# Optimization experiments

Hardware: AMD Instinct MI355X
Metric: run time of the kernel (lower is better)

## Reference

```python
import jax, jax.numpy as jnp
import numpy as np

HRNN = 2e-11  # seconds per step; t grid is in nanoseconds (x1e9), step = 0.02
W0, W1 = -20.0, 10.0          # fixed oscillator coupling weights
X0 = (0.4736, 0.8745, 1.8497)  # fixed initial state


def setup_inputs() -> dict:
    key = jax.random.key(0)
    ks = jax.random.split(key, 9)
    B, T, NIN, NHI, NHO, NOUT = 1024, 2048, 8, 64, 64, 1
    g = lambda k, shape, s: jax.random.normal(k, shape, jnp.float32) * s
    return {
        "inputdata": jax.random.normal(ks[0], (B, T, NIN), jnp.float32),
        "Wni": g(ks[1], (NHI, NIN), 1.0 / np.sqrt(NIN)),   # nonlinearinput
        "bni": g(ks[2], (NHI,), 0.1),
        "Wli": g(ks[3], (1, NHI), 1.0 / np.sqrt(NHI)),     # linearinput
        "bli": g(ks[4], (1,), 0.1),
        "tau": jnp.zeros((1,), jnp.float32),                # nn.Parameter(Tensor(1))
        "Wn": g(ks[5], (NHO, 3), 1.0 / np.sqrt(3.0)),      # nonlinear readout
        "bn": g(ks[6], (NHO,), 0.1),
        "Wl": g(ks[7], (NOUT, NHO), 1.0 / np.sqrt(NHO)),   # linear readout
        "bl": g(ks[8], (NOUT,), 0.1),
    }


def reference(inputdata, Wni, bni, Wli, bli, tau, Wn, bn, Wl, bl):
    B, T, NIN = inputdata.shape
    tg = jnp.linspace(0.0, HRNN * (T - 1) * 1e9, T).astype(jnp.float32)
    u = inputdata  # [B, T, NIN]
    x0 = jnp.broadcast_to(jnp.array(X0, jnp.float32)[None, :], (B, 3))

    def lin_interp(t):
        # clamp-to-edge linear interpolation of u along the time grid
        ind = jnp.clip(jnp.searchsorted(tg, t), 1, T - 1)
        t_lo, t_hi = tg[ind - 1], tg[ind]
        frac = jnp.clip((t - t_lo) / (t_hi - t_lo), 0.0, 1.0)
        u_lo = u[:, ind - 1, :]
        return u_lo + (u[:, ind, :] - u_lo) * frac  # [B, NIN]

    def f(t, x):
        ut = lin_interp(t)
        dparam = jax.nn.sigmoid(ut @ Wni.T + bni) @ Wli.T + bli  # [B, 1]
        tx = jnp.tanh(x)
        dx = jnp.stack(
            (-x[:, 0] + tx[:, 1],
             -x[:, 1] + tx[:, 2],
             -x[:, 2] + W0 * tx[:, 0] + W1 * tx[:, 1]),
            axis=1,
        )
        return dx / jnp.exp(tau + dparam)  # [B, 3]

    def step(x, ts):
        # torchdiffeq 'rk4' = fourth-order 3/8 rule between grid points
        t0, t1 = ts
        h = t1 - t0
        k1 = f(t0, x)
        k2 = f(t0 + h / 3, x + h * k1 / 3)
        k3 = f(t0 + 2 * h / 3, x + h * (k2 - k1 / 3))
        k4 = f(t1, x + h * (k1 - k2 + k3))
        xn = x + h * (k1 + 3 * k2 + 3 * k3 + k4) / 8
        return xn, xn

    _, xs = jax.lax.scan(step, x0, (tg[:-1], tg[1:]))  # [T-1, B, 3]
    outrnn = jnp.concatenate([x0[None], xs], axis=0).transpose(1, 0, 2)  # [B, T, 3]
    hid = jax.nn.sigmoid(outrnn @ Wn.T + bn)  # [B, T, NHO]
    return hid @ Wl.T + bl  # [B, T, NOUT]
```

## Files before the change

### kernel.cpp

```cpp
#include <hip/hip_runtime.h>

#define BB 1024
#define TT 2048
#define NIN 8
#define NHI 64

#define CS 2.8853900817779268f
#define NL2E 1.4426950408889634f
#define DELTA (40.94f / 2047.0f)

__device__ __forceinline__ float sig_pre(float zs) {
    float e = __builtin_amdgcn_exp2f(zs);
    return __builtin_amdgcn_rcpf(1.0f + e);
}

template<int CTRL>
__device__ __forceinline__ float qperm(float x) {
    int r = __builtin_amdgcn_mov_dpp(__float_as_int(x), CTRL, 0xF, 0xF, true);
    return __int_as_float(r);
}

__global__ __launch_bounds__(256) void precompute_r(
    const float* __restrict__ u, const float* __restrict__ Wni,
    const float* __restrict__ bni, const float* __restrict__ Wli,
    const float* __restrict__ bli, const float* __restrict__ tau,
    float* __restrict__ r3)
{
    __shared__ float sWni[NHI * NIN];
    __shared__ float sbni[NHI];
    __shared__ float sWli[NHI];
    int lt = threadIdx.x;
    for (int i = lt; i < NHI * NIN; i += 256) sWni[i] = Wni[i] * -NL2E;
    if (lt < NHI) { sbni[lt] = bni[lt] * -NL2E; sWli[lt] = Wli[lt]; }
    __syncthreads();

    int lane = lt & 63;
    long long gw = (long long)blockIdx.x * 4 + (lt >> 6);
    int b = (int)(gw / 33);
    int chunk = (int)(gw % 33);
    int s = chunk * 63 + lane;
    int sc = s < TT ? s : TT - 1;

    const float4* up4 = reinterpret_cast<const float4*>(u + ((long long)b * TT + sc) * NIN);
    float4 uA = up4[0], uB = up4[1];

    float d0 = 0.f, d1 = 0.f, d2 = 0.f;
    #pragma unroll 8
    for (int j = 0; j < NHI; j++) {
        const float* wj = &sWni[j * NIN];
        float z = sbni[j];
        z = fmaf(wj[0], uA.x, z); z = fmaf(wj[1], uA.y, z);
        z = fmaf(wj[2], uA.z, z); z = fmaf(wj[3], uA.w, z);
        z = fmaf(wj[4], uB.x, z); z = fmaf(wj[5], uB.y, z);
        z = fmaf(wj[6], uB.z, z); z = fmaf(wj[7], uB.w, z);
        float zn = __shfl_down(z, 1);
        float dz = zn - z;
        float z1 = fmaf(dz, 1.0f / 3.0f, z);
        float z2 = fmaf(dz, 2.0f / 3.0f, z);
        float wl = sWli[j];
        d0 = fmaf(wl, sig_pre(z),  d0);
        d1 = fmaf(wl, sig_pre(z1), d1);
        d2 = fmaf(wl, sig_pre(z2), d2);
    }
    float base = tau[0] + bli[0];
    float r0 = __builtin_amdgcn_exp2f((base + d0) * -NL2E);
    float r1 = __builtin_amdgcn_exp2f((base + d1) * -NL2E);
    float r2 = __builtin_amdgcn_exp2f((base + d2) * -NL2E);

    if (s < TT) {
        float* p = r3 + ((long long)b * TT + s) * 3;
        p[0] = r0;
        if (lane < 63 && s < TT - 1) { p[1] = r1; p[2] = r2; }
    }
}

__global__ __launch_bounds__(64) void scan_kernel(
    const float* __restrict__ r3, float* __restrict__ xs)
{
    int gt = blockIdx.x * 64 + threadIdx.x;
    int b = gt >> 2;
    int l = gt & 3;

    const float4* rp = reinterpret_cast<const float4*>(r3 + (long long)b * TT * 3);
    float* xp3 = xs + (long long)b * TT * 3;

    const float h = DELTA;
    bool is2 = (l == 2);
    float cA = is2 ? 40.0f * CS : -2.0f * CS;
    float cB = is2 ? -20.0f * CS : 0.0f;
    float Kl = is2 ? -10.0f * CS : CS;

    float X = (l == 0) ? 0.4736f * CS : (is2 ? 1.8497f * CS : 0.8745f * CS);
    if (l < 3) xp3[l] = X * (1.0f / CS);

#define QSTAGE(Xin, Wout) \
    { float e_ = __builtin_amdgcn_exp2f(Xin); \
      float r_ = __builtin_amdgcn_rcpf(1.0f + e_); \
      float p1_ = qperm<0x89>(r_); \
      float p2_ = qperm<0x10>(r_); \
      Wout = fmaf(cA, p1_, fmaf(cB, p2_, Kl - (Xin))); }

#define STEP(sidx, R1v, R2v, R3v, R4v) do { \
    float hr1 = h * (R1v), hr2 = h * (R2v), hr3 = h * (R3v); \
    float q1 = hr1 * (1.0f / 3.0f); \
    float a1 = hr1 * 0.125f, a2 = hr2 * 0.375f, a3 = hr3 * 0.375f; \
    float hr4_8 = (h * (R4v)) * 0.125f; \
    float W1, W2, W3, W4; \
    QSTAGE(X, W1); \
    float A  = fmaf(q1, W1, X); \
    float AC = fmaf(a1, W1, X); \
    float Q3 = fmaf(-q1, W1, X); \
    float U4 = fmaf(hr1, W1, X); \
    QSTAGE(A, W2); \
    float Bv = fmaf(hr2, W2, Q3); \
    float Q4 = fmaf(-hr2, W2, U4); \
    AC = fmaf(a2, W2, AC); \
    QSTAGE(Bv, W3); \
    float Cv = fmaf(hr3, W3, Q4); \
    AC = fmaf(a3, W3, AC); \
    QSTAGE(Cv, W4); \
    X = fmaf(hr4_8, W4, AC); \
    if (l < 3) xp3[(long long)((sidx) + 1) * 3 + l] = X * (1.0f / CS); \
} while (0)

    float4 f0 = rp[0], f1 = rp[1], f2 = rp[2];
    float4 n0 = rp[3], n1 = rp[4], n2 = rp[5];

    for (int j = 0; j < 510; j++) {
        float4 m0 = rp[3 * j + 6], m1 = rp[3 * j + 7], m2 = rp[3 * j + 8];
        int s4 = 4 * j;
        STEP(s4 + 0, f0.x, f0.y, f0.z, f0.w);
        STEP(s4 + 1, f0.w, f1.x, f1.y, f1.z);
        STEP(s4 + 2, f1.z, f1.w, f2.x, f2.y);
        STEP(s4 + 3, f2.y, f2.z, f2.w, n0.x);
        f0 = n0; f1 = n1; f2 = n2;
        n0 = m0; n1 = m1; n2 = m2;
    }
    STEP(2040, f0.x, f0.y, f0.z, f0.w);
    STEP(2041, f0.w, f1.x, f1.y, f1.z);
    STEP(2042, f1.z, f1.w, f2.x, f2.y);
    STEP(2043, f2.y, f2.z, f2.w, n0.x);
    f0 = n0; f1 = n1; f2 = n2;
    STEP(2044, f0.x, f0.y, f0.z, f0.w);
    STEP(2045, f0.w, f1.x, f1.y, f1.z);
    STEP(2046, f1.z, f1.w, f2.x, f2.y);
#undef STEP
#undef QSTAGE
}

__global__ __launch_bounds__(256) void out_kernel(
    const float* __restrict__ xs, const float* __restrict__ Wn,
    const float* __restrict__ bn, const float* __restrict__ Wl,
    const float* __restrict__ bl, float* __restrict__ out)
{
    __shared__ float sWn[NHI * 3];
    __shared__ float sbn[NHI];
    __shared__ float sWl[NHI];
    int lt = threadIdx.x;
    if (lt < NHI * 3) sWn[lt] = Wn[lt] * -NL2E;
    if (lt < NHI) { sbn[lt] = bn[lt] * -NL2E; sWl[lt] = Wl[lt]; }
    __syncthreads();

    long long tid = (long long)blockIdx.x * 256 + lt;
    const float* xpt = xs + tid * 3;
    float c0 = xpt[0], c1 = xpt[1], c2 = xpt[2];
    float acc = 0.0f;
    #pragma unroll 8
    for (int j = 0; j < NHI; j++) {
        float z = fmaf(sWn[j * 3], c0,
                  fmaf(sWn[j * 3 + 1], c1,
                  fmaf(sWn[j * 3 + 2], c2, sbn[j])));
        acc = fmaf(sWl[j], sig_pre(z), acc);
    }
    out[tid] = acc + bl[0];
}

extern "C" void kernel_launch(void* const* d_in, const int* in_sizes, int n_in,
                              void* d_out, int out_size, void* d_ws, size_t ws_size,
                              hipStream_t stream) {
    const float* u    = (const float*)d_in[0];
    const float* Wni  = (const float*)d_in[1];
    const float* bni  = (const float*)d_in[2];
    const float* Wli  = (const float*)d_in[3];
    const float* bli  = (const float*)d_in[4];
    const float* tau  = (const float*)d_in[5];
    const float* Wn   = (const float*)d_in[6];
    const float* bn   = (const float*)d_in[7];
    const float* Wl   = (const float*)d_in[8];
    const float* bl   = (const float*)d_in[9];
    float* out = (float*)d_out;

    float* r3 = (float*)d_ws;
    float* xs = r3 + (size_t)3 * BB * TT;

    precompute_r<<<(BB * 33) / 4, 256, 0, stream>>>(u, Wni, bni, Wli, bli, tau, r3);
    scan_kernel<<<(BB * 4) / 64, 64, 0, stream>>>(r3, xs);
    out_kernel<<<(BB * TT) / 256, 256, 0, stream>>>(xs, Wn, bn, Wl, bl, out);
}
```

Baseline: 455.7 us.

## Restructure RK stage dependency chain and store scan states as planar float4

```diff
diff --git a/kernel.cpp b/kernel.cpp
--- a/kernel.cpp
+++ b/kernel.cpp
@@ -6,6 +6,7 @@
 #define NHI 64
 
 #define CS 2.8853900817779268f
+#define ICS (1.0f / CS)
 #define NL2E 1.4426950408889634f
 #define DELTA (40.94f / 2047.0f)
 
@@ -82,7 +83,8 @@
     int l = gt & 3;
 
     const float4* rp = reinterpret_cast<const float4*>(r3 + (long long)b * TT * 3);
-    float* xp3 = xs + (long long)b * TT * 3;
+    int comp = (l == 3) ? 1 : l;
+    float* xc = xs + (long long)comp * BB * TT + (long long)b * TT;
 
     const float h = DELTA;
     bool is2 = (l == 2);
@@ -91,36 +93,50 @@
     float Kl = is2 ? -10.0f * CS : CS;
 
     float X = (l == 0) ? 0.4736f * CS : (is2 ? 1.8497f * CS : 0.8745f * CS);
-    if (l < 3) xp3[l] = X * (1.0f / CS);
-
-#define QSTAGE(Xin, Wout) \
-    { float e_ = __builtin_amdgcn_exp2f(Xin); \
-      float r_ = __builtin_amdgcn_rcpf(1.0f + e_); \
-      float p1_ = qperm<0x89>(r_); \
-      float p2_ = qperm<0x10>(r_); \
-      Wout = fmaf(cA, p1_, fmaf(cB, p2_, Kl - (Xin))); }
-
-#define STEP(sidx, R1v, R2v, R3v, R4v) do { \
-    float hr1 = h * (R1v), hr2 = h * (R2v), hr3 = h * (R3v); \
-    float q1 = hr1 * (1.0f / 3.0f); \
-    float a1 = hr1 * 0.125f, a2 = hr2 * 0.375f, a3 = hr3 * 0.375f; \
-    float hr4_8 = (h * (R4v)) * 0.125f; \
-    float W1, W2, W3, W4; \
-    QSTAGE(X, W1); \
-    float A  = fmaf(q1, W1, X); \
-    float AC = fmaf(a1, W1, X); \
-    float Q3 = fmaf(-q1, W1, X); \
-    float U4 = fmaf(hr1, W1, X); \
-    QSTAGE(A, W2); \
-    float Bv = fmaf(hr2, W2, Q3); \
-    float Q4 = fmaf(-hr2, W2, U4); \
-    AC = fmaf(a2, W2, AC); \
-    QSTAGE(Bv, W3); \
-    float Cv = fmaf(hr3, W3, Q4); \
-    AC = fmaf(a3, W3, AC); \
-    QSTAGE(Cv, W4); \
-    X = fmaf(hr4_8, W4, AC); \
-    if (l < 3) xp3[(long long)((sidx) + 1) * 3 + l] = X * (1.0f / CS); \
+
+#define STEP(R1v, R2v, R3v, R4v) do { \
+    float g1 = h * (R1v), g2 = h * (R2v), g3 = h * (R3v); \
+    float q  = g1 * (1.0f / 3.0f); \
+    float g4_8 = (h * (R4v)) * 0.125f; \
+    float cA1 = q * cA,    cB1 = q * cB; \
+    float cA2 = g2 * cA,   cB2 = g2 * cB; \
+    float cA3 = g3 * cA,   cB3 = g3 * cB; \
+    float cA4 = g4_8 * cA, cB4 = g4_8 * cB; \
+     \
+    float e1 = __builtin_amdgcn_exp2f(X); \
+    float rho1 = __builtin_amdgcn_rcpf(1.0f + e1); \
+    float KmX = Kl - X; \
+    float pb2 = fmaf(q, KmX, X); \
+    float p11 = qperm<0x89>(rho1), p21 = qperm<0x10>(rho1); \
+    float S2 = fmaf(cA1, p11, fmaf(cB1, p21, pb2)); \
+    float V1 = fmaf(cA, p11, cB * p21); \
+    float W1 = V1 + KmX; \
+     \
+    float e2 = __builtin_amdgcn_exp2f(S2); \
+    float rho2 = __builtin_amdgcn_rcpf(1.0f + e2); \
+    float KmS2 = Kl - S2; \
+    float pb3 = fmaf(g2, KmS2, fmaf(-q, W1, X)); \
+    float p12 = qperm<0x89>(rho2), p22 = qperm<0x10>(rho2); \
+    float S3 = fmaf(cA2, p12, fmaf(cB2, p22, pb3)); \
+    float V2 = fmaf(cA, p12, cB * p22); \
+    float W2 = V2 + KmS2; \
+     \
+    float e3 = __builtin_amdgcn_exp2f(S3); \
+    float rho3 = __builtin_amdgcn_rcpf(1.0f + e3); \
+    float KmS3 = Kl - S3; \
+    float pb4 = fmaf(g3, KmS3, fmaf(-g2, W2, fmaf(g1, W1, X))); \
+    float p13 = qperm<0x89>(rho3), p23 = qperm<0x10>(rho3); \
+    float S4 = fmaf(cA3, p13, fmaf(cB3, p23, pb4)); \
+    float V3 = fmaf(cA, p13, cB * p23); \
+    float W3 = V3 + KmS3; \
+     \
+    float e4 = __builtin_amdgcn_exp2f(S4); \
+    float rho4 = __builtin_amdgcn_rcpf(1.0f + e4); \
+    float KmS4 = Kl - S4; \
+    float t3 = fmaf(3.0f * g3, W3, fmaf(3.0f * g2, W2, g1 * W1)); \
+    float pbX = fmaf(g4_8, KmS4, fmaf(0.125f, t3, X)); \
+    float p14 = qperm<0x89>(rho4), p24 = qperm<0x10>(rho4); \
+    X = fmaf(cA4, p14, fmaf(cB4, p24, pbX)); \
 } while (0)
 
     float4 f0 = rp[0], f1 = rp[1], f2 = rp[2];
@@ -128,24 +144,35 @@
 
     for (int j = 0; j < 510; j++) {
         float4 m0 = rp[3 * j + 6], m1 = rp[3 * j + 7], m2 = rp[3 * j + 8];
-        int s4 = 4 * j;
-        STEP(s4 + 0, f0.x, f0.y, f0.z, f0.w);
-        STEP(s4 + 1, f0.w, f1.x, f1.y, f1.z);
-        STEP(s4 + 2, f1.z, f1.w, f2.x, f2.y);
-        STEP(s4 + 3, f2.y, f2.z, f2.w, n0.x);
+        float4 ov;
+        ov.x = X * ICS;
+        STEP(f0.x, f0.y, f0.z, f0.w);  ov.y = X * ICS;
+        STEP(f0.w, f1.x, f1.y, f1.z);  ov.z = X * ICS;
+        STEP(f1.z, f1.w, f2.x, f2.y);  ov.w = X * ICS;
+        *reinterpret_cast<float4*>(xc + 4 * j) = ov;
+        STEP(f2.y, f2.z, f2.w, n0.x);
         f0 = n0; f1 = n1; f2 = n2;
         n0 = m0; n1 = m1; n2 = m2;
     }
-    STEP(2040, f0.x, f0.y, f0.z, f0.w);
-    STEP(2041, f0.w, f1.x, f1.y, f1.z);
-    STEP(2042, f1.z, f1.w, f2.x, f2.y);
-    STEP(2043, f2.y, f2.z, f2.w, n0.x);
-    f0 = n0; f1 = n1; f2 = n2;
-    STEP(2044, f0.x, f0.y, f0.z, f0.w);
-    STEP(2045, f0.w, f1.x, f1.y, f1.z);
-    STEP(2046, f1.z, f1.w, f2.x, f2.y);
+    {
+        float4 ov;
+        ov.x = X * ICS;
+        STEP(f0.x, f0.y, f0.z, f0.w);  ov.y = X * ICS;
+        STEP(f0.w, f1.x, f1.y, f1.z);  ov.z = X * ICS;
+        STEP(f1.z, f1.w, f2.x, f2.y);  ov.w = X * ICS;
+        *reinterpret_cast<float4*>(xc + 4 * 510) = ov;
+        STEP(f2.y, f2.z, f2.w, n0.x);
+        f0 = n0; f1 = n1; f2 = n2;
+    }
+    {
+        float4 ov;
+        ov.x = X * ICS;
+        STEP(f0.x, f0.y, f0.z, f0.w);  ov.y = X * ICS;
+        STEP(f0.w, f1.x, f1.y, f1.z);  ov.z = X * ICS;
+        STEP(f1.z, f1.w, f2.x, f2.y);  ov.w = X * ICS;
+        *reinterpret_cast<float4*>(xc + 4 * 511) = ov;
+    }
 #undef STEP
-#undef QSTAGE
 }
 
 __global__ __launch_bounds__(256) void out_kernel(
@@ -162,8 +189,9 @@
     __syncthreads();
 
     long long tid = (long long)blockIdx.x * 256 + lt;
-    const float* xpt = xs + tid * 3;
-    float c0 = xpt[0], c1 = xpt[1], c2 = xpt[2];
+    float c0 = xs[tid];
+    float c1 = xs[(long long)BB * TT + tid];
+    float c2 = xs[(long long)2 * BB * TT + tid];
     float acc = 0.0f;
     #pragma unroll 8
     for (int j = 0; j < NHI; j++) {
```

Result: faster. 437.9 us (-3.9%).
